# Kernel optimization log

Hardware: AMD Instinct MI355X
Metric: run time of the kernel (lower is better)

Reference implementation:

```python
import jax, jax.numpy as jnp
import numpy as np

BS = 32  # leaf block size


def setup_inputs() -> dict:
    key = jax.random.key(0)
    ks = jax.random.split(key, 10)
    N, C, E, H = 262144, 128, 4194304, 4
    x = jax.random.normal(ks[0], (1, N, C), jnp.float32)
    rows = jax.random.randint(ks[1], (E,), 0, N, dtype=jnp.int32)
    offs = jax.random.randint(ks[2], (E,), -16, 16, dtype=jnp.int32)
    cols = jnp.clip(rows + offs, 0, N - 1)
    edge_index = jnp.stack([rows, cols], axis=0)  # (2, E) int32
    edge_values = jax.random.normal(ks[3], (E,), jnp.float32)
    positions = jax.random.uniform(ks[4], (N, 3), jnp.float32)
    qkv_w = jax.random.normal(ks[5], (C, 3 * C), jnp.float32) * 0.02
    qkv_b = jnp.zeros((3 * C,), jnp.float32)
    proj_w = jax.random.normal(ks[6], (C, C), jnp.float32) * 0.02
    proj_b = jnp.zeros((C,), jnp.float32)
    gate_w = jax.random.normal(ks[7], (H, 1), jnp.float32) * 0.01  # nn.Linear(1, H)
    gate_b = jnp.zeros((H,), jnp.float32)
    return {"x": x, "edge_index": edge_index, "edge_values": edge_values,
            "positions": positions, "qkv_w": qkv_w, "qkv_b": qkv_b,
            "proj_w": proj_w, "proj_b": proj_b, "gate_w": gate_w, "gate_b": gate_b}


def _build_leaf_block_connectivity(edge_index, edge_values, positions, num_blocks, dtype):
    # Returns attn_mask (nb, 32, 33) and edge_feats (nb, 32, 33, 4) = (dx,dy,dz,w).
    rows, cols = edge_index[0], edge_index[1]
    br, bc = rows // BS, cols // BS
    in_blk = (br == bc) & (br < num_blocks)
    b_safe = jnp.where(in_blk, br, num_blocks)  # out-of-block edges -> dummy block
    rl, cl = rows % BS, cols % BS
    dx = positions[cols] - positions[rows]               # (E, 3)
    ef_flat = jnp.concatenate([dx, edge_values[:, None]], axis=1).astype(dtype)  # (E, 4)
    diag = jnp.arange(BS)
    attn_mask = jnp.zeros((num_blocks + 1, BS, BS + 1), dtype)
    attn_mask = attn_mask.at[:, diag, diag].set(1.0)      # self
    attn_mask = attn_mask.at[:, :, BS].set(1.0)           # block node
    attn_mask = attn_mask.at[b_safe, rl, cl].set(1.0)     # edges
    edge_feats = jnp.zeros((num_blocks + 1, BS, BS + 1, 4), dtype)
    edge_feats = edge_feats.at[b_safe, rl, cl].set(ef_flat)
    return attn_mask[:num_blocks], edge_feats[:num_blocks]


def reference(x, edge_index, edge_values, positions, qkv_w, qkv_b, proj_w, proj_b, gate_w, gate_b):
    B, N, C = x.shape
    H = gate_b.shape[0]
    hd = C // H
    scale = hd ** -0.5
    nb = N // BS
    dtype = x.dtype
    attn_mask, edge_feats = _build_leaf_block_connectivity(edge_index, edge_values, positions, nb, dtype)

    x_blk = x.reshape(B, nb, BS, C)
    block_node = x_blk.mean(axis=2, keepdims=True)            # (B, nb, 1, C)
    kv = jnp.concatenate([x_blk, block_node], axis=2)          # (B, nb, 33, C)
    qkv_q = x_blk @ qkv_w + qkv_b
    qkv_kv = kv @ qkv_w + qkv_b
    q = qkv_q[..., :C].reshape(B, nb, BS, H, hd)
    k = qkv_kv[..., C:2 * C].reshape(B, nb, BS + 1, H, hd)
    v = qkv_kv[..., 2 * C:].reshape(B, nb, BS + 1, H, hd)

    scores = jnp.einsum('bnqhd,bnkhd->bnqkh', q, k) * scale    # (B, nb, 32, 33, H)

    diag = jnp.arange(BS)
    w_bias = edge_feats[..., 3]                                # (nb, 32, 33)
    w_bias = w_bias.at[:, :, BS].set(1.0)
    w_bias = w_bias.at[:, diag, diag].set(1.0)
    scores = scores + w_bias[None, :, :, :, None]

    mask = attn_mask[None, :, :, :, None]                      # (1, nb, 32, 33, 1)
    neg = jnp.asarray(-1e9, dtype)
    scores = jnp.where(mask == 0, neg, scores)
    attn_probs = jax.nn.softmax(scores, axis=3)

    # edge_gate: Linear(1, H) applied to w_bias, zeroed where masked, added post-softmax
    gate = w_bias[..., None] * gate_w[:, 0] + gate_b           # (nb, 32, 33, H)
    gate = jnp.where(mask[0] == 0, 0.0, gate)[None]            # (1, nb, 32, 33, H)
    combined = attn_probs + gate

    out = jnp.einsum('bnqkh,bnkhd->bnqhd', combined, v).reshape(B, N, C)
    return out @ proj_w + proj_b
```

## Files before the change

kernel.cpp:

```cpp
#include <hip/hip_runtime.h>
#include <hip/hip_bf16.h>

#define BS 32
#define NBC 33

typedef unsigned long long ull;
typedef __attribute__((ext_vector_type(8))) __bf16 bf16x8;
typedef __attribute__((ext_vector_type(4))) float f32x4;
typedef __attribute__((ext_vector_type(4))) unsigned short us4;

__device__ __forceinline__ unsigned short f2b(float f) {
    __hip_bfloat16 h = __float2bfloat16(f);
    return *reinterpret_cast<unsigned short*>(&h);
}
__device__ __forceinline__ float b2f(unsigned short u) {
    union { unsigned int i; float f; } x; x.i = ((unsigned int)u) << 16; return x.f;
}
#define LD8(p) (*reinterpret_cast<const bf16x8*>(p))

#define ZB 2048
__global__ void zero_prepack_kernel(uint4* __restrict__ tbl4, int n4,
                                    const float* __restrict__ qkv_w,
                                    const float* __restrict__ proj_w,
                                    unsigned short* __restrict__ wq,
                                    unsigned short* __restrict__ wp) {
    if (blockIdx.x < ZB) {
        int stride = ZB * 256;
        for (int i = blockIdx.x * 256 + threadIdx.x; i < n4; i += stride)
            tbl4[i] = make_uint4(0u, 0u, 0u, 0u);
    } else {
        int tid = (blockIdx.x - ZB) * 256 + threadIdx.x;
        int f = tid >> 9, lane = (tid >> 3) & 63, j = tid & 7;
        int ks = f & 3;
        int kk = ks * 32 + (lane >> 4) * 8 + j;
        int nn = lane & 15;
        if (f < 96) {
            int t = f >> 2;
            int w = t / 6, s = t % 6;
            int g = (s < 2) ? (2 * w + s) : (s < 4) ? (8 + 2 * w + (s - 2)) : (16 + 2 * w + (s - 4));
            wq[tid] = f2b(qkv_w[kk * 384 + g * 16 + nn]);
        } else {
            int f2 = f - 96;
            wp[f2 * 512 + lane * 8 + j] = f2b(proj_w[kk * 128 + (f2 >> 2) * 16 + nn]);
        }
    }
}

__global__ void edge_scatter_kernel(const int* __restrict__ rows,
                                    const int* __restrict__ cols,
                                    const float* __restrict__ vals,
                                    ull* __restrict__ tbl, int E) {
    int base = (blockIdx.x * 256 + threadIdx.x) * 4;
    if (base >= E) return;
    if (base + 4 <= E) {
        int4 r4 = *reinterpret_cast<const int4*>(rows + base);
        int4 c4 = *reinterpret_cast<const int4*>(cols + base);
        float4 v4 = *reinterpret_cast<const float4*>(vals + base);
        int rr[4] = {r4.x, r4.y, r4.z, r4.w};
        int cc[4] = {c4.x, c4.y, c4.z, c4.w};
        float vv[4] = {v4.x, v4.y, v4.z, v4.w};
        #pragma unroll
        for (int k = 0; k < 4; ++k) {
            int r = rr[k], c = cc[k];
            if ((r >> 5) == (c >> 5) && r != c) {
                ull key = ((ull)(unsigned)(base + k + 1) << 32) | (ull)__float_as_uint(vv[k]);
                atomicMax(&tbl[((size_t)(r >> 5) * BS + (r & 31)) * NBC + (c & 31)], key);
            }
        }
    } else {
        for (int e = base; e < E && e < base + 4; ++e) {
            int r = rows[e], c = cols[e];
            if ((r >> 5) == (c >> 5) && r != c) {
                ull key = ((ull)(unsigned)(e + 1) << 32) | (ull)__float_as_uint(vals[e]);
                atomicMax(&tbl[((size_t)(r >> 5) * BS + (r & 31)) * NBC + (c & 31)], key);
            }
        }
    }
}

__global__ __launch_bounds__(512)
void block_attn_kernel(const float* __restrict__ x,
                       const ull* __restrict__ tbl,
                       const unsigned short* __restrict__ wq,
                       const unsigned short* __restrict__ wp,
                       const float* __restrict__ qkv_b,
                       const float* __restrict__ proj_b,
                       const float* __restrict__ gate_w,
                       const float* __restrict__ gate_b,
                       float* __restrict__ out) {
    __shared__ __align__(16) unsigned char smem[31040];
    unsigned short (*qs)[32][40]  = (unsigned short (*)[32][40])(smem);
    unsigned short (*ksm)[33][40] = (unsigned short (*)[33][40])(smem + 10240);
    unsigned short (*vT)[32][40]  = (unsigned short (*)[32][40])(smem + 20800);
    unsigned short (*xs)[136]     = (unsigned short (*)[136])(smem + 20800);

    const int b = blockIdx.x, t = threadIdx.x;
    const int h = (t >> 6) & 3, half = t >> 8;
    const int l = t & 63, g16 = l >> 4, c16 = l & 15;
    const f32x4 z4 = {0.f, 0.f, 0.f, 0.f};
    const float NEG = -1.0e30f;

    const float* xb = x + (size_t)b * (BS * 128);
    #pragma unroll
    for (int it = 0; it < 2; ++it) {
        int idx = (t + it * 512) * 4;
        float4 v = *reinterpret_cast<const float4*>(xb + idx);
        us4 u; u.x = f2b(v.x); u.y = f2b(v.y); u.z = f2b(v.z); u.w = f2b(v.w);
        *reinterpret_cast<us4*>(&xs[idx >> 7][idx & 127]) = u;
    }

    float wb[4][3];
    {
        const ull* tb = tbl + (size_t)b * (BS * NBC);
        #pragma unroll
        for (int r = 0; r < 4; ++r) {
            const int i = 16 * half + 4 * g16 + r;
            #pragma unroll
            for (int nt = 0; nt < 2; ++nt) {
                const int j = 16 * nt + c16;
                const ull wv = tb[i * NBC + j];
                wb[r][nt] = (j == i) ? 1.f
                           : (wv ? __uint_as_float((unsigned)(wv & 0xffffffffu)) : NEG);
            }
            wb[r][2] = (c16 == 0) ? 1.f : NEG;
        }
    }
    __syncthreads();

    bf16x8 a[2][4];
    #pragma unroll
    for (int mt = 0; mt < 2; ++mt)
        #pragma unroll
        for (int ks = 0; ks < 4; ++ks)
            a[mt][ks] = LD8(&xs[c16 + 16 * mt][ks * 32 + g16 * 8]);
    __syncthreads();

    {
        const unsigned short* wqs = wq + (size_t)(h * 24) * 512 + l * 8;
        #pragma unroll
        for (int si = 0; si < 3; ++si) {
            const int s = 2 * si + half;
            bf16x8 bn[4];
            #pragma unroll
            for (int ks = 0; ks < 4; ++ks) bn[ks] = LD8(wqs + (s * 4 + ks) * 512);
            f32x4 acc0 = z4, acc1 = z4;
            __builtin_amdgcn_s_setprio(1);
            #pragma unroll
            for (int ks = 0; ks < 4; ++ks) {
                acc0 = __builtin_amdgcn_mfma_f32_16x16x32_bf16(a[0][ks], bn[ks], acc0, 0, 0, 0);
                acc1 = __builtin_amdgcn_mfma_f32_16x16x32_bf16(a[1][ks], bn[ks], acc1, 0, 0, 0);
            }
            __builtin_amdgcn_s_setprio(0);
            const float bias = qkv_b[si * 128 + 32 * h + 16 * half + c16];
            const int cc = 16 * half + c16;
            if (si == 0) {
                #pragma unroll
                for (int r = 0; r < 4; ++r) {
                    qs[h][4 * g16 + r][cc]      = f2b(acc0[r] + bias);
                    qs[h][16 + 4 * g16 + r][cc] = f2b(acc1[r] + bias);
                }
            } else {
                float csum = acc0[0] + acc0[1] + acc0[2] + acc0[3]
                           + acc1[0] + acc1[1] + acc1[2] + acc1[3];
                csum += __shfl_xor(csum, 16, 64);
                csum += __shfl_xor(csum, 32, 64);
                const float meanv = csum * (1.f / 32.f) + bias;
                if (si == 1) {
                    #pragma unroll
                    for (int r = 0; r < 4; ++r) {
                        ksm[h][4 * g16 + r][cc]      = f2b(acc0[r] + bias);
                        ksm[h][16 + 4 * g16 + r][cc] = f2b(acc1[r] + bias);
                    }
                    if (g16 == 0) ksm[h][32][cc] = f2b(meanv);
                } else {
                    #pragma unroll
                    for (int r = 0; r < 4; ++r) {
                        vT[h][cc][4 * g16 + r]      = f2b(acc0[r] + bias);
                        vT[h][cc][16 + 4 * g16 + r] = f2b(acc1[r] + bias);
                    }
                    if (g16 == 0) vT[h][cc][32] = f2b(meanv);
                }
            }
        }
    }
    __syncthreads();

    f32x4 sS[3];
    {
        bf16x8 aq  = LD8(&qs[h][16 * half + c16][g16 * 8]);
        bf16x8 bk0 = LD8(&ksm[h][c16][g16 * 8]);
        bf16x8 bk1 = LD8(&ksm[h][16 + c16][g16 * 8]);
        bf16x8 bk2 = LD8(&ksm[h][32][g16 * 8]);
        bf16x8 zb;
        #pragma unroll
        for (int q = 0; q < 8; ++q) zb[q] = (__bf16)0.f;
        if (c16 != 0) bk2 = zb;
        __builtin_amdgcn_s_setprio(1);
        sS[0] = __builtin_amdgcn_mfma_f32_16x16x32_bf16(aq, bk0, z4, 0, 0, 0);
        sS[1] = __builtin_amdgcn_mfma_f32_16x16x32_bf16(aq, bk1, z4, 0, 0, 0);
        sS[2] = __builtin_amdgcn_mfma_f32_16x16x32_bf16(aq, bk2, z4, 0, 0, 0);
        __builtin_amdgcn_s_setprio(0);
    }

    {
        const float scale = 0.17677669529663687f;
        const float gwh = gate_w[h], gbh = gate_b[h];
        #pragma unroll
        for (int r = 0; r < 4; ++r) {
            const int i = 16 * half + 4 * g16 + r;
            float sc[3];
            #pragma unroll
            for (int k = 0; k < 3; ++k) sc[k] = sS[k][r] * scale + wb[r][k];
            float mx = fmaxf(fmaxf(sc[0], sc[1]), sc[2]);
            mx = fmaxf(mx, __shfl_xor(mx, 1, 64));
            mx = fmaxf(mx, __shfl_xor(mx, 2, 64));
            mx = fmaxf(mx, __shfl_xor(mx, 4, 64));
            mx = fmaxf(mx, __shfl_xor(mx, 8, 64));
            float e0 = __expf(sc[0] - mx), e1 = __expf(sc[1] - mx), e2 = __expf(sc[2] - mx);
            float sum = e0 + e1 + e2;
            sum += __shfl_xor(sum, 1, 64);
            sum += __shfl_xor(sum, 2, 64);
            sum += __shfl_xor(sum, 4, 64);
            sum += __shfl_xor(sum, 8, 64);
            const float inv = __builtin_amdgcn_rcpf(sum);
            float gt0 = (wb[r][0] > -1.0e29f) ? wb[r][0] * gwh + gbh : 0.f;
            float gt1 = (wb[r][1] > -1.0e29f) ? wb[r][1] * gwh + gbh : 0.f;
            float gt2 = (wb[r][2] > -1.0e29f) ? gwh + gbh : 0.f;
            qs[h][i][c16]      = f2b(e0 * inv + gt0);
            qs[h][i][16 + c16] = f2b(e1 * inv + gt1);
            if (c16 == 0) vT[h][i][33] = f2b(e2 * inv + gt2);
        }
    }

    {
        bf16x8 ap = LD8(&qs[h][16 * half + c16][g16 * 8]);
        f32x4 o[2];
        __builtin_amdgcn_s_setprio(1);
        #pragma unroll
        for (int nt = 0; nt < 2; ++nt) {
            bf16x8 bv = LD8(&vT[h][16 * nt + c16][g16 * 8]);
            o[nt] = __builtin_amdgcn_mfma_f32_16x16x32_bf16(ap, bv, z4, 0, 0, 0);
        }
        __builtin_amdgcn_s_setprio(0);
        #pragma unroll
        for (int nt = 0; nt < 2; ++nt) {
            const float vm = b2f(vT[h][16 * nt + c16][32]);
            #pragma unroll
            for (int r = 0; r < 4; ++r)
                o[nt][r] += b2f(vT[h][16 * half + 4 * g16 + r][33]) * vm;
        }
        #pragma unroll
        for (int nt = 0; nt < 2; ++nt)
            #pragma unroll
            for (int r = 0; r < 4; ++r)
                qs[h][16 * half + 4 * g16 + r][16 * nt + c16] = f2b(o[nt][r]);
    }
    __syncthreads();

    {
        const int ct = t >> 6;
        bf16x8 aa[2][4];
        #pragma unroll
        for (int mt = 0; mt < 2; ++mt)
            #pragma unroll
            for (int hh = 0; hh < 4; ++hh)
                aa[mt][hh] = LD8(&qs[hh][c16 + 16 * mt][g16 * 8]);
        f32x4 po[2];
        po[0] = z4; po[1] = z4;
        const unsigned short* wps = wp + l * 8;
        bf16x8 bw0 = LD8(wps + (size_t)(ct * 4 + 0) * 512);
        bf16x8 bw1 = LD8(wps + (size_t)(ct * 4 + 1) * 512);
        bf16x8 bw2 = LD8(wps + (size_t)(ct * 4 + 2) * 512);
        bf16x8 bw3 = LD8(wps + (size_t)(ct * 4 + 3) * 512);
        __builtin_amdgcn_s_setprio(1);
        po[0] = __builtin_amdgcn_mfma_f32_16x16x32_bf16(aa[0][0], bw0, po[0], 0, 0, 0);
        po[1] = __builtin_amdgcn_mfma_f32_16x16x32_bf16(aa[1][0], bw0, po[1], 0, 0, 0);
        po[0] = __builtin_amdgcn_mfma_f32_16x16x32_bf16(aa[0][1], bw1, po[0], 0, 0, 0);
        po[1] = __builtin_amdgcn_mfma_f32_16x16x32_bf16(aa[1][1], bw1, po[1], 0, 0, 0);
        po[0] = __builtin_amdgcn_mfma_f32_16x16x32_bf16(aa[0][2], bw2, po[0], 0, 0, 0);
        po[1] = __builtin_amdgcn_mfma_f32_16x16x32_bf16(aa[1][2], bw2, po[1], 0, 0, 0);
        po[0] = __builtin_amdgcn_mfma_f32_16x16x32_bf16(aa[0][3], bw3, po[0], 0, 0, 0);
        po[1] = __builtin_amdgcn_mfma_f32_16x16x32_bf16(aa[1][3], bw3, po[1], 0, 0, 0);
        __builtin_amdgcn_s_setprio(0);
        float* ob = out + (size_t)b * (BS * 128);
        const int col = 16 * ct + c16;
        const float pbv = proj_b[col];
        #pragma unroll
        for (int mt = 0; mt < 2; ++mt)
            #pragma unroll
            for (int r = 0; r < 4; ++r)
                ob[(size_t)(16 * mt + 4 * g16 + r) * 128 + col] = po[mt][r] + pbv;
    }
}

extern "C" void kernel_launch(void* const* d_in, const int* in_sizes, int n_in,
                              void* d_out, int out_size, void* d_ws, size_t ws_size,
                              hipStream_t stream) {
    const float* x      = (const float*)d_in[0];
    const int*   ei     = (const int*)d_in[1];
    const float* ev     = (const float*)d_in[2];
    const float* qkv_w  = (const float*)d_in[4];
    const float* qkv_b  = (const float*)d_in[5];
    const float* proj_w = (const float*)d_in[6];
    const float* proj_b = (const float*)d_in[7];
    const float* gate_w = (const float*)d_in[8];
    const float* gate_b = (const float*)d_in[9];
    float* out = (float*)d_out;

    const int E  = in_sizes[2];
    const int N  = in_sizes[0] / 128;
    const int nb = N / BS;

    ull* tbl = (ull*)d_ws;
    size_t twords = (size_t)nb * BS * NBC;
    size_t tbytes = (twords * sizeof(ull) + 255) & ~(size_t)255;
    unsigned short* wqp = (unsigned short*)((char*)d_ws + tbytes);
    unsigned short* wpp = wqp + 96 * 512;

    zero_prepack_kernel<<<ZB + 256, 256, 0, stream>>>((uint4*)tbl,
                                                      (int)(twords * sizeof(ull) / 16),
                                                      qkv_w, proj_w, wqp, wpp);
    edge_scatter_kernel<<<((E + 3) / 4 + 255) / 256, 256, 0, stream>>>(ei, ei + E, ev, tbl, E);
    block_attn_kernel<<<nb, 512, 0, stream>>>(x, tbl, wqp, wpp, qkv_b, proj_b,
                                              gate_w, gate_b, out);
}
```

Baseline: 261.3 us.

## Shrink edge table to 32-bit with two-pass index-then-value scatter

The 64-bit packed (index, value) atomicMax table is replaced by a 32-bit table. A first pass atomically records the largest edge index per cell, and a second pass lets the winning edge overwrite its cell with its float value. This halves the memory the zeroing kernel writes and the attention kernel reads; the attention kernel now stages its per-block slice into LDS. In exchange, the edge arrays are read a second time with extra random cell accesses and one more kernel launch. The encoding also treats a winning value of exactly 0.0f as a missing edge.

```diff
diff --git a/kernel.cpp b/kernel.cpp
--- a/kernel.cpp
+++ b/kernel.cpp
@@ -46,10 +46,37 @@
     }
 }
 
-__global__ void edge_scatter_kernel(const int* __restrict__ rows,
-                                    const int* __restrict__ cols,
-                                    const float* __restrict__ vals,
-                                    ull* __restrict__ tbl, int E) {
+__global__ void edge_scatter1_kernel(const int* __restrict__ rows,
+                                     const int* __restrict__ cols,
+                                     unsigned* __restrict__ tbl, int E) {
+    int base = (blockIdx.x * 256 + threadIdx.x) * 4;
+    if (base >= E) return;
+    if (base + 4 <= E) {
+        int4 r4 = *reinterpret_cast<const int4*>(rows + base);
+        int4 c4 = *reinterpret_cast<const int4*>(cols + base);
+        int rr[4] = {r4.x, r4.y, r4.z, r4.w};
+        int cc[4] = {c4.x, c4.y, c4.z, c4.w};
+        #pragma unroll
+        for (int k = 0; k < 4; ++k) {
+            int r = rr[k], c = cc[k];
+            if ((r >> 5) == (c >> 5) && r != c)
+                atomicMax(&tbl[((size_t)(r >> 5) * BS + (r & 31)) * NBC + (c & 31)],
+                          (unsigned)(base + k + 1));
+        }
+    } else {
+        for (int e = base; e < E && e < base + 4; ++e) {
+            int r = rows[e], c = cols[e];
+            if ((r >> 5) == (c >> 5) && r != c)
+                atomicMax(&tbl[((size_t)(r >> 5) * BS + (r & 31)) * NBC + (c & 31)],
+                          (unsigned)(e + 1));
+        }
+    }
+}
+
+__global__ void edge_scatter2_kernel(const int* __restrict__ rows,
+                                     const int* __restrict__ cols,
+                                     const float* __restrict__ vals,
+                                     unsigned* __restrict__ tbl, int E) {
     int base = (blockIdx.x * 256 + threadIdx.x) * 4;
     if (base >= E) return;
     if (base + 4 <= E) {
@@ -63,16 +90,16 @@
         for (int k = 0; k < 4; ++k) {
             int r = rr[k], c = cc[k];
             if ((r >> 5) == (c >> 5) && r != c) {
-                ull key = ((ull)(unsigned)(base + k + 1) << 32) | (ull)__float_as_uint(vv[k]);
-                atomicMax(&tbl[((size_t)(r >> 5) * BS + (r & 31)) * NBC + (c & 31)], key);
+                unsigned* cell = &tbl[((size_t)(r >> 5) * BS + (r & 31)) * NBC + (c & 31)];
+                if (*cell == (unsigned)(base + k + 1)) *cell = __float_as_uint(vv[k]);
             }
         }
     } else {
         for (int e = base; e < E && e < base + 4; ++e) {
             int r = rows[e], c = cols[e];
             if ((r >> 5) == (c >> 5) && r != c) {
-                ull key = ((ull)(unsigned)(e + 1) << 32) | (ull)__float_as_uint(vals[e]);
-                atomicMax(&tbl[((size_t)(r >> 5) * BS + (r & 31)) * NBC + (c & 31)], key);
+                unsigned* cell = &tbl[((size_t)(r >> 5) * BS + (r & 31)) * NBC + (c & 31)];
+                if (*cell == (unsigned)(e + 1)) *cell = __float_as_uint(vals[e]);
             }
         }
     }
@@ -80,7 +107,7 @@
 
 __global__ __launch_bounds__(512)
 void block_attn_kernel(const float* __restrict__ x,
-                       const ull* __restrict__ tbl,
+                       const unsigned* __restrict__ tbl,
                        const unsigned short* __restrict__ wq,
                        const unsigned short* __restrict__ wp,
                        const float* __restrict__ qkv_b,
@@ -88,11 +115,12 @@
                        const float* __restrict__ gate_w,
                        const float* __restrict__ gate_b,
                        float* __restrict__ out) {
-    __shared__ __align__(16) unsigned char smem[31040];
+    __shared__ __align__(16) unsigned char smem[35264];
     unsigned short (*qs)[32][40]  = (unsigned short (*)[32][40])(smem);
     unsigned short (*ksm)[33][40] = (unsigned short (*)[33][40])(smem + 10240);
     unsigned short (*vT)[32][40]  = (unsigned short (*)[32][40])(smem + 20800);
     unsigned short (*xs)[136]     = (unsigned short (*)[136])(smem + 20800);
+    unsigned* etab                = (unsigned*)(smem + 31040);
 
     const int b = blockIdx.x, t = threadIdx.x;
     const int h = (t >> 6) & 3, half = t >> 8;
@@ -108,24 +136,24 @@
         us4 u; u.x = f2b(v.x); u.y = f2b(v.y); u.z = f2b(v.z); u.w = f2b(v.w);
         *reinterpret_cast<us4*>(&xs[idx >> 7][idx & 127]) = u;
     }
+    if (t < 264) {
+        const uint4* tb4 = reinterpret_cast<const uint4*>(tbl + (size_t)b * (BS * NBC));
+        reinterpret_cast<uint4*>(etab)[t] = tb4[t];
+    }
+    __syncthreads();
 
     float wb[4][3];
-    {
-        const ull* tb = tbl + (size_t)b * (BS * NBC);
-        #pragma unroll
-        for (int r = 0; r < 4; ++r) {
-            const int i = 16 * half + 4 * g16 + r;
-            #pragma unroll
-            for (int nt = 0; nt < 2; ++nt) {
-                const int j = 16 * nt + c16;
-                const ull wv = tb[i * NBC + j];
-                wb[r][nt] = (j == i) ? 1.f
-                           : (wv ? __uint_as_float((unsigned)(wv & 0xffffffffu)) : NEG);
-            }
-            wb[r][2] = (c16 == 0) ? 1.f : NEG;
-        }
-    }
-    __syncthreads();
+    #pragma unroll
+    for (int r = 0; r < 4; ++r) {
+        const int i = 16 * half + 4 * g16 + r;
+        #pragma unroll
+        for (int nt = 0; nt < 2; ++nt) {
+            const int j = 16 * nt + c16;
+            const unsigned u = etab[i * NBC + j];
+            wb[r][nt] = (j == i) ? 1.f : (u ? __uint_as_float(u) : NEG);
+        }
+        wb[r][2] = (c16 == 0) ? 1.f : NEG;
+    }
 
     bf16x8 a[2][4];
     #pragma unroll
@@ -311,16 +339,18 @@
     const int N  = in_sizes[0] / 128;
     const int nb = N / BS;
 
-    ull* tbl = (ull*)d_ws;
+    unsigned* tbl = (unsigned*)d_ws;
     size_t twords = (size_t)nb * BS * NBC;
-    size_t tbytes = (twords * sizeof(ull) + 255) & ~(size_t)255;
+    size_t tbytes = (twords * sizeof(unsigned) + 255) & ~(size_t)255;
     unsigned short* wqp = (unsigned short*)((char*)d_ws + tbytes);
     unsigned short* wpp = wqp + 96 * 512;
 
     zero_prepack_kernel<<<ZB + 256, 256, 0, stream>>>((uint4*)tbl,
-                                                      (int)(twords * sizeof(ull) / 16),
+                                                      (int)(twords * sizeof(unsigned) / 16),
                                                       qkv_w, proj_w, wqp, wpp);
-    edge_scatter_kernel<<<((E + 3) / 4 + 255) / 256, 256, 0, stream>>>(ei, ei + E, ev, tbl, E);
+    int sgrid = ((E + 3) / 4 + 255) / 256;
+    edge_scatter1_kernel<<<sgrid, 256, 0, stream>>>(ei, ei + E, tbl, E);
+    edge_scatter2_kernel<<<sgrid, 256, 0, stream>>>(ei, ei + E, ev, tbl, E);
     block_attn_kernel<<<nb, 512, 0, stream>>>(x, tbl, wqp, wpp, qkv_b, proj_b,
                                               gate_w, gate_b, out);
 }
```

Result: slower. 342.5 us (+31.1%).
